# Optimization experiments

Measured on AMD Instinct MI355X. Metric: run time of the kernel, lower is better.

## Reference

```python
import jax, jax.numpy as jnp
import numpy as np

EMBED = 768
HEADS = 12
HEAD_DIM = EMBED // HEADS
RATES = (1, 2, 4)
SEGS = (2048, 4096, 8192)


def setup_inputs() -> dict:
    key = jax.random.key(0)
    k1, k2, k3 = jax.random.split(key, 3)
    b, n = 2, 8192
    x = jax.random.normal(k1, (b, n, EMBED), dtype=jnp.float32)
    Wqkv = jax.random.normal(k2, (3 * EMBED, EMBED), dtype=jnp.float32) * 0.02
    Wout = jax.random.normal(k3, (EMBED, EMBED), dtype=jnp.float32) * 0.02
    return {"x": x, "Wqkv": Wqkv, "Wout": Wout}


def _dilated_attention(qkv):
    # qkv: [b, n, 3, h, d]
    b, n, _, h, d = qkv.shape
    scale = 1.0 / jnp.sqrt(jnp.asarray(d, qkv.dtype))
    out = jnp.zeros((b, n, h, d), dtype=qkv.dtype)
    for r, s in zip(RATES, SEGS):
        sr = s // r
        nseg = n // s
        # strided gather: [b, nseg, sr, 3, h, d]
        g = qkv.reshape(b, nseg, s, 3, h, d)[:, :, ::r]
        # fold stride offset into batch; attention runs over the segment axis
        g = g.transpose(0, 2, 1, 3, 4, 5).reshape(b * sr, nseg, 3, h, d)
        q, k, v = g[:, :, 0], g[:, :, 1], g[:, :, 2]
        scores = jnp.einsum('bnhd,bmhd->bhnm', q, k) * scale
        attn = jax.nn.softmax(scores, axis=-1)
        o = jnp.einsum('bhnm,bmhd->bnhd', attn, v)
        # scatter-add back into strided positions
        o = o.reshape(b, sr, nseg, h, d).transpose(0, 2, 1, 3, 4)
        out = out.reshape(b, nseg, s, h, d).at[:, :, ::r].add(o).reshape(b, n, h, d)
    # normalize over full sequence dim (as in original module)
    out = out / out.sum(axis=1, keepdims=True)
    return out


def reference(x, Wqkv, Wout):
    b, n, e = x.shape
    qkv = (x @ Wqkv.T).reshape(b, n, 3, HEADS, HEAD_DIM)
    o = _dilated_attention(qkv)  # [b, n, h, d]
    return o.reshape(b, n, e) @ Wout.T
```

## Files before the change

### kernel.cpp

```cpp
#include <hip/hip_runtime.h>

typedef unsigned short u16;
typedef __attribute__((ext_vector_type(8))) short bf16x8;
typedef __attribute__((ext_vector_type(4))) float f32x4;

__device__ __forceinline__ u16 f2bf_rne(float f) {
  unsigned u = __float_as_uint(f);
  u += 0x7fffu + ((u >> 16) & 1u);
  return (u16)(u >> 16);
}
__device__ __forceinline__ float bf2f(u16 h) {
  return __uint_as_float(((unsigned)h) << 16);
}
__device__ __forceinline__ void split1(float v, u16& h, u16& l) {
  u16 hh = f2bf_rne(v);
  h = hh;
  l = f2bf_rne(v - bf2f(hh));
}

__device__ __forceinline__ void gl16(const void* g, void* l) {
  __builtin_amdgcn_global_load_lds(
      (const __attribute__((address_space(1))) unsigned int*)g,
      (__attribute__((address_space(3))) unsigned int*)l,
      16, 0, 0);
}

__global__ void split_convert_all(const float4* __restrict__ x,
                                  ushort4* __restrict__ xhi, ushort4* __restrict__ xlo,
                                  const float4* __restrict__ wq,
                                  ushort4* __restrict__ wqh, ushort4* __restrict__ wql) {
  int i = blockIdx.x * 256 + threadIdx.x;
  const float4* src;
  ushort4 *dh, *dl;
  int idx;
  if (i < 3145728) { src = x; dh = xhi; dl = xlo; idx = i; }
  else if (i < 3588096) { src = wq; dh = wqh; dl = wql; idx = i - 3145728; }
  else return;
  float4 v = src[idx];
  ushort4 h, l;
  split1(v.x, h.x, l.x); split1(v.y, h.y, l.y);
  split1(v.z, h.z, l.z); split1(v.w, h.w, l.w);
  dh[idx] = h; dl[idx] = l;
}

template <int BM, bool SPLIT>
__global__ __launch_bounds__(256, (BM == 128 ? 2 : 3)) void gemm_split_bt(
    const u16* __restrict__ Ahi, const u16* __restrict__ Alo, int lda,
    const u16* __restrict__ Bhi, const u16* __restrict__ Blo,
    const u16* __restrict__ Bhi2, const u16* __restrict__ Blo2,
    void* __restrict__ Cv, int M, int N, int K) {
  constexpr int MI = BM / 32;
  constexpr int AR = BM / 4;
  constexpr int RA = AR / 8;
  __shared__ __align__(16) u16 sAh[BM * 64], sAl[BM * 64];
  __shared__ __align__(16) u16 sBh[128 * 64], sBl[128 * 64];
  const int tid = threadIdx.x;
  const int wave = tid >> 6;
  const int lane = tid & 63;
  const int tm0 = blockIdx.x * BM;
  const int tn0 = blockIdx.y * 128;
  const int wm = (wave & 1) * (BM / 2);
  const int wn = (wave >> 1) * 64;
  if (2 * tm0 >= M) { Bhi = Bhi2; Blo = Blo2; }

  const int c = lane & 7;
  const int scol = (c ^ ((lane >> 3) & 7)) * 8;
  const int srowA = wave * AR + (lane >> 3);
  const int srowB = wave * 32 + (lane >> 3);
  const u16* gAh = Ahi + (size_t)(tm0 + srowA) * lda + scol;
  const u16* gAl = Alo + (size_t)(tm0 + srowA) * lda + scol;
  const u16* gBh = Bhi + (size_t)(tn0 + srowB) * K + scol;
  const u16* gBl = Blo + (size_t)(tn0 + srowB) * K + scol;
  u16* lAh = &sAh[wave * AR * 64];
  u16* lAl = &sAl[wave * AR * 64];
  u16* lBh = &sBh[wave * 32 * 64];
  u16* lBl = &sBl[wave * 32 * 64];
  const size_t rstepA = (size_t)8 * lda;
  const size_t rstepB = (size_t)8 * K;

  f32x4 acc[MI][4] = {};
  const int fr = lane & 15;
  const int quad = lane >> 4;

  for (int kt = 0; kt < K; kt += 64) {
#pragma unroll
    for (int r = 0; r < 4; ++r) {
      if (r < RA) {
        gl16(gAh + kt + r * rstepA, lAh + r * 512);
        gl16(gAl + kt + r * rstepA, lAl + r * 512);
      }
      gl16(gBh + kt + r * rstepB, lBh + r * 512);
      gl16(gBl + kt + r * rstepB, lBl + r * 512);
    }
    __syncthreads();
    for (int subk = 0; subk < 2; ++subk) {
      const int k0 = ((subk * 4 + quad) ^ (fr & 7)) * 8;
      bf16x8 ah[MI], al[MI], bh[4], bl[4];
#pragma unroll
      for (int i = 0; i < MI; ++i) {
        ah[i] = *(const bf16x8*)&sAh[(wm + i * 16 + fr) * 64 + k0];
        al[i] = *(const bf16x8*)&sAl[(wm + i * 16 + fr) * 64 + k0];
      }
#pragma unroll
      for (int j = 0; j < 4; ++j) {
        bh[j] = *(const bf16x8*)&sBh[(wn + j * 16 + fr) * 64 + k0];
        bl[j] = *(const bf16x8*)&sBl[(wn + j * 16 + fr) * 64 + k0];
      }
#pragma unroll
      for (int i = 0; i < MI; ++i)
#pragma unroll
        for (int j = 0; j < 4; ++j) {
          acc[i][j] = __builtin_amdgcn_mfma_f32_16x16x32_bf16(ah[i], bh[j], acc[i][j], 0, 0, 0);
          acc[i][j] = __builtin_amdgcn_mfma_f32_16x16x32_bf16(ah[i], bl[j], acc[i][j], 0, 0, 0);
          acc[i][j] = __builtin_amdgcn_mfma_f32_16x16x32_bf16(al[i], bh[j], acc[i][j], 0, 0, 0);
        }
    }
    __syncthreads();
  }

  const int col = lane & 15;
  const int rowq = (lane >> 4) * 4;
  if (SPLIT) {
    u16* Cs = (u16*)Cv;
#pragma unroll
    for (int i = 0; i < MI; ++i)
#pragma unroll
      for (int j = 0; j < 4; ++j) {
        const int n = tn0 + wn + j * 16 + col;
        size_t base = (size_t)(tm0 + wm + i * 16 + rowq) * 4608 + n;
#pragma unroll
        for (int r = 0; r < 4; ++r) {
          u16 h, l;
          split1(acc[i][j][r], h, l);
          Cs[base + (size_t)r * 4608] = h;
          Cs[base + (size_t)r * 4608 + 2304] = l;
        }
      }
  } else {
    float* C = (float*)Cv;
#pragma unroll
    for (int i = 0; i < MI; ++i)
#pragma unroll
      for (int j = 0; j < 4; ++j) {
        size_t base = (size_t)(tm0 + wm + i * 16 + rowq) * N + (tn0 + wn + j * 16 + col);
#pragma unroll
        for (int r = 0; r < 4; ++r) C[base + (size_t)r * N] = acc[i][j][r];
      }
  }
}

__global__ __launch_bounds__(256) void attn_dilated(const u16* __restrict__ qks,
                                                    u16* __restrict__ qk16,
                                                    float* __restrict__ Spart) {
  __shared__ float rows[4][2312];
  __shared__ float sc[12][16];
  __shared__ float Aw[12][16];
  const int t = threadIdx.x;
  const int i0 = blockIdx.x;
  const int b = blockIdx.y;
  const size_t rowbase = (size_t)b * 8192 + i0;

  for (int idx = t; idx < 4 * 576; idx += 256) {
    int j = idx / 576, c4 = idx - j * 576;
    const u16* slot = qks + (rowbase + 2048 * j) * 4608;
    ushort4 h = ((const ushort4*)slot)[c4];
    ushort4 l = ((const ushort4*)(slot + 2304))[c4];
    float4 v;
    v.x = bf2f(h.x) + bf2f(l.x);
    v.y = bf2f(h.y) + bf2f(l.y);
    v.z = bf2f(h.z) + bf2f(l.z);
    v.w = bf2f(h.w) + bf2f(l.w);
    ((float4*)rows[j])[c4] = v;
  }
  __syncthreads();

  if (t < 192) {
    int h = t >> 4, j = (t >> 2) & 3, jp = t & 3;
    const float4* q = (const float4*)&rows[j][h * 64];
    const float4* k = (const float4*)&rows[jp][768 + h * 64];
    float s = 0.f;
#pragma unroll
    for (int d = 0; d < 16; ++d) {
      float4 a = q[d], bb = k[d];
      s += a.x * bb.x + a.y * bb.y + a.z * bb.z + a.w * bb.w;
    }
    sc[h][(j << 2) | jp] = s * 0.125f;
  }
  __syncthreads();

  if (t < 48) {
    int h = t >> 2, j = t & 3;
    float s0 = sc[h][j * 4 + 0], s1 = sc[h][j * 4 + 1];
    float s2 = sc[h][j * 4 + 2], s3 = sc[h][j * 4 + 3];
    float m = fmaxf(fmaxf(s0, s1), fmaxf(s2, s3));
    float e0 = expf(s0 - m), e1 = expf(s1 - m), e2 = expf(s2 - m), e3 = expf(s3 - m);
    float inv = 1.f / (e0 + e1 + e2 + e3);
    float a[4] = {e0 * inv, e1 * inv, e2 * inv, e3 * inv};
    if ((i0 & 1) == 0) {
      int p = j ^ 2;
      float ss = sc[h][j * 4 + j], sx = sc[h][j * 4 + p];
      float mm = fmaxf(ss, sx);
      float es = expf(ss - mm), ex = expf(sx - mm);
      float iv = 1.f / (es + ex);
      a[j] += es * iv;
      a[p] += ex * iv;
    }
    if ((i0 & 3) == 0) a[j] += 1.f;
    Aw[h][j * 4 + 0] = a[0]; Aw[h][j * 4 + 1] = a[1];
    Aw[h][j * 4 + 2] = a[2]; Aw[h][j * 4 + 3] = a[3];
  }
  __syncthreads();

  float* sp = Spart + ((size_t)b * 64 + (i0 & 63)) * 768;
#pragma unroll
  for (int rep = 0; rep < 3; ++rep) {
    int cc = rep * 256 + t;
    int h = cc >> 6;
    float ps = 0.f;
#pragma unroll
    for (int j = 0; j < 4; ++j) {
      float v = 0.f;
#pragma unroll
      for (int jp = 0; jp < 4; ++jp) v = fmaf(Aw[h][(j << 2) | jp], rows[jp][1536 + cc], v);
      u16 h16, l16;
      split1(v, h16, l16);
      size_t base = (rowbase + 2048 * j) * 4608;
      qk16[base + cc] = h16;
      qk16[base + 768 + cc] = l16;
      ps += v;
    }
    atomicAdd(&sp[cc], ps);
  }
}

__global__ void colred(const float* __restrict__ Spart, float* __restrict__ Sinv) {
  int i = blockIdx.x * 256 + threadIdx.x;
  if (i >= 1536) return;
  int b = i / 768, c = i - b * 768;
  const float* p = Spart + (size_t)b * 64 * 768 + c;
  float s = 0.f;
#pragma unroll
  for (int g = 0; g < 64; ++g) s += p[g * 768];
  Sinv[i] = 1.0f / s;
}

__global__ void scale_wout(const float4* __restrict__ Wout, const float* __restrict__ Sinv,
                           ushort4* __restrict__ wh0, ushort4* __restrict__ wl0,
                           ushort4* __restrict__ wh1, ushort4* __restrict__ wl1) {
  int i = blockIdx.x * 256 + threadIdx.x;
  if (i >= 294912) return;
  int b = i / 147456;
  int r = i - b * 147456;
  int c = (r % 192) * 4;
  const float* s = Sinv + b * 768 + c;
  float4 v = Wout[r];
  v.x *= s[0]; v.y *= s[1]; v.z *= s[2]; v.w *= s[3];
  ushort4 h, l;
  split1(v.x, h.x, l.x); split1(v.y, h.y, l.y);
  split1(v.z, h.z, l.z); split1(v.w, h.w, l.w);
  if (b == 0) { wh0[r] = h; wl0[r] = l; }
  else        { wh1[r] = h; wl1[r] = l; }
}

extern "C" void kernel_launch(void* const* d_in, const int* in_sizes, int n_in,
                              void* d_out, int out_size, void* d_ws, size_t ws_size,
                              hipStream_t stream) {
  (void)in_sizes; (void)n_in; (void)out_size; (void)ws_size;
  const float* x = (const float*)d_in[0];
  const float* Wqkv = (const float*)d_in[1];
  const float* Wout = (const float*)d_in[2];
  float* out = (float*)d_out;

  char* w = (char*)d_ws;
  u16* qk16 = (u16*)(w);
  size_t off = 150994944;
  u16* xhi = (u16*)(w + off);
  float* Spart = (float*)(w + off);
  float* Sinv = (float*)(w + off + 393216);
  u16* wh0 = (u16*)(w + off + 400000);
  u16* wl0 = (u16*)(w + off + 1579648);
  u16* wh1 = (u16*)(w + off + 2759296);
  u16* wl1 = (u16*)(w + off + 3938944);
  off += 25165824;
  u16* xlo = (u16*)(w + off); off += 25165824;
  u16* wqh = (u16*)(w + off); off += 3538944;
  u16* wql = (u16*)(w + off); off += 3538944;

  split_convert_all<<<dim3(14016), 256, 0, stream>>>(
      (const float4*)x, (ushort4*)xhi, (ushort4*)xlo,
      (const float4*)Wqkv, (ushort4*)wqh, (ushort4*)wql);

  gemm_split_bt<128, true><<<dim3(128, 18), 256, 0, stream>>>(
      xhi, xlo, 768, wqh, wql, wqh, wql, qk16, 16384, 2304, 768);

  hipMemsetAsync(Spart, 0, 393216, stream);
  attn_dilated<<<dim3(2048, 2), 256, 0, stream>>>(qk16, qk16, Spart);

  colred<<<dim3(6), 256, 0, stream>>>(Spart, Sinv);

  scale_wout<<<dim3(1152), 256, 0, stream>>>((const float4*)Wout, Sinv,
                                             (ushort4*)wh0, (ushort4*)wl0,
                                             (ushort4*)wh1, (ushort4*)wl1);

  gemm_split_bt<64, false><<<dim3(256, 6), 256, 0, stream>>>(
      qk16, qk16 + 768, 4608, wh0, wl0, wh1, wl1, out, 16384, 768, 768);
}
```

Baseline: 367.9 us.

## Split dilated attention kernel into per-head-pair single-wave blocks

```diff
diff --git a/kernel.cpp b/kernel.cpp
--- a/kernel.cpp
+++ b/kernel.cpp
@@ -2,6 +2,7 @@
 
 typedef unsigned short u16;
 typedef __attribute__((ext_vector_type(8))) short bf16x8;
+typedef __attribute__((ext_vector_type(8))) unsigned short u16x8;
 typedef __attribute__((ext_vector_type(4))) float f32x4;
 
 __device__ __forceinline__ u16 f2bf_rne(float f) {
@@ -149,47 +150,60 @@
   }
 }
 
-__global__ __launch_bounds__(256) void attn_dilated(const u16* __restrict__ qks,
-                                                    u16* __restrict__ qk16,
-                                                    float* __restrict__ Spart) {
-  __shared__ float rows[4][2312];
-  __shared__ float sc[12][16];
-  __shared__ float Aw[12][16];
-  const int t = threadIdx.x;
+__global__ __launch_bounds__(64) void attn_dilated(const u16* __restrict__ qks,
+                                                   u16* __restrict__ qk16,
+                                                   float* __restrict__ Spart) {
+  __shared__ float f[1536];
+  __shared__ float sc[2][16];
+  __shared__ float Aw[2][16];
+  const int lane = threadIdx.x;
   const int i0 = blockIdx.x;
   const int b = blockIdx.y;
+  const int hp = blockIdx.z;
   const size_t rowbase = (size_t)b * 8192 + i0;
 
-  for (int idx = t; idx < 4 * 576; idx += 256) {
-    int j = idx / 576, c4 = idx - j * 576;
+#pragma unroll
+  for (int it = 0; it < 3; ++it) {
+    int item = it * 64 + lane;
+    int j = item / 48, rem = item - j * 48;
+    int seg = rem >> 4, chunk = rem & 15;
     const u16* slot = qks + (rowbase + 2048 * j) * 4608;
-    ushort4 h = ((const ushort4*)slot)[c4];
-    ushort4 l = ((const ushort4*)(slot + 2304))[c4];
-    float4 v;
-    v.x = bf2f(h.x) + bf2f(l.x);
-    v.y = bf2f(h.y) + bf2f(l.y);
-    v.z = bf2f(h.z) + bf2f(l.z);
-    v.w = bf2f(h.w) + bf2f(l.w);
-    ((float4*)rows[j])[c4] = v;
+    const u16* p = slot + seg * 768 + hp * 128 + chunk * 8;
+    u16x8 h8 = *(const u16x8*)p;
+    u16x8 l8 = *(const u16x8*)(p + 2304);
+    float4 v0, v1;
+    v0.x = bf2f(h8[0]) + bf2f(l8[0]);
+    v0.y = bf2f(h8[1]) + bf2f(l8[1]);
+    v0.z = bf2f(h8[2]) + bf2f(l8[2]);
+    v0.w = bf2f(h8[3]) + bf2f(l8[3]);
+    v1.x = bf2f(h8[4]) + bf2f(l8[4]);
+    v1.y = bf2f(h8[5]) + bf2f(l8[5]);
+    v1.z = bf2f(h8[6]) + bf2f(l8[6]);
+    v1.w = bf2f(h8[7]) + bf2f(l8[7]);
+    float* dst = &f[j * 384 + seg * 128 + chunk * 8];
+    ((float4*)dst)[0] = v0;
+    ((float4*)dst)[1] = v1;
   }
   __syncthreads();
 
-  if (t < 192) {
-    int h = t >> 4, j = (t >> 2) & 3, jp = t & 3;
-    const float4* q = (const float4*)&rows[j][h * 64];
-    const float4* k = (const float4*)&rows[jp][768 + h * 64];
+  {
+    int half = lane >> 5, l5 = lane & 31;
+    int h = l5 >> 4, j = (l5 >> 2) & 3, jp = l5 & 3;
+    const float4* q = (const float4*)&f[j * 384 + h * 64 + half * 32];
+    const float4* k = (const float4*)&f[jp * 384 + 128 + h * 64 + half * 32];
     float s = 0.f;
 #pragma unroll
-    for (int d = 0; d < 16; ++d) {
+    for (int d = 0; d < 8; ++d) {
       float4 a = q[d], bb = k[d];
       s += a.x * bb.x + a.y * bb.y + a.z * bb.z + a.w * bb.w;
     }
-    sc[h][(j << 2) | jp] = s * 0.125f;
+    s += __shfl_xor(s, 32);
+    if (half == 0) sc[h][(j << 2) | jp] = s * 0.125f;
   }
   __syncthreads();
 
-  if (t < 48) {
-    int h = t >> 2, j = t & 3;
+  if (lane < 8) {
+    int h = lane >> 2, j = lane & 3;
     float s0 = sc[h][j * 4 + 0], s1 = sc[h][j * 4 + 1];
     float s2 = sc[h][j * 4 + 2], s3 = sc[h][j * 4 + 3];
     float m = fmaxf(fmaxf(s0, s1), fmaxf(s2, s3));
@@ -211,22 +225,28 @@
   }
   __syncthreads();
 
-  float* sp = Spart + ((size_t)b * 64 + (i0 & 63)) * 768;
-#pragma unroll
-  for (int rep = 0; rep < 3; ++rep) {
-    int cc = rep * 256 + t;
+  float* sp = Spart + ((size_t)b * 64 + (i0 & 63)) * 768 + hp * 128;
+#pragma unroll
+  for (int it = 0; it < 2; ++it) {
+    int cc = it * 64 + lane;
     int h = cc >> 6;
+    float v0 = f[0 * 384 + 256 + cc];
+    float v1 = f[1 * 384 + 256 + cc];
+    float v2 = f[2 * 384 + 256 + cc];
+    float v3 = f[3 * 384 + 256 + cc];
     float ps = 0.f;
 #pragma unroll
     for (int j = 0; j < 4; ++j) {
       float v = 0.f;
-#pragma unroll
-      for (int jp = 0; jp < 4; ++jp) v = fmaf(Aw[h][(j << 2) | jp], rows[jp][1536 + cc], v);
+      v = fmaf(Aw[h][(j << 2) | 0], v0, v);
+      v = fmaf(Aw[h][(j << 2) | 1], v1, v);
+      v = fmaf(Aw[h][(j << 2) | 2], v2, v);
+      v = fmaf(Aw[h][(j << 2) | 3], v3, v);
       u16 h16, l16;
       split1(v, h16, l16);
       size_t base = (rowbase + 2048 * j) * 4608;
-      qk16[base + cc] = h16;
-      qk16[base + 768 + cc] = l16;
+      qk16[base + 1536 + hp * 128 + cc] = h16;
+      qk16[base + 3840 + hp * 128 + cc] = l16;
       ps += v;
     }
     atomicAdd(&sp[cc], ps);
@@ -294,7 +314,7 @@
       xhi, xlo, 768, wqh, wql, wqh, wql, qk16, 16384, 2304, 768);
 
   hipMemsetAsync(Spart, 0, 393216, stream);
-  attn_dilated<<<dim3(2048, 2), 256, 0, stream>>>(qk16, qk16, Spart);
+  attn_dilated<<<dim3(2048, 2, 6), 64, 0, stream>>>(qk16, qk16, Spart);
 
   colred<<<dim3(6), 256, 0, stream>>>(Spart, Sinv);
 
@@ -303,5 +323,5 @@
                                              (ushort4*)wh1, (ushort4*)wl1);
 
   gemm_split_bt<64, false><<<dim3(256, 6), 256, 0, stream>>>(
-      qk16, qk16 + 768, 4608, wh0, wl0, wh1, wl1, out, 16384, 768, 768);
-}
+      qk16 + 1536, qk16 + 3840, 4608, wh0, wl0, wh1, wl1, out, 16384, 768, 768);
+}
```

Result: slower. 375.7 us (+2.1%).
